# Kernel optimization log

Hardware: AMD Instinct MI355X
Metric: run time of the kernel (lower is better)

## Reference

```python
import jax, jax.numpy as jnp
import numpy as np

L, DIM = 8192, 2048

def setup_inputs() -> dict:
    key = jax.random.key(0)
    k1, k2, k3, k4 = jax.random.split(key, 4)
    x = jax.random.normal(k1, (L, DIM), dtype=jnp.float32)
    x_mix_last = jax.random.normal(k2, (DIM,), dtype=jnp.float32)
    factor_param = jax.random.uniform(k3, (DIM,), dtype=jnp.float32)
    W = jax.random.normal(k4, (DIM, DIM), dtype=jnp.float32) * 0.02
    return {"x": x, "x_mix_last": x_mix_last, "factor_param": factor_param, "W": W}

def reference(x, x_mix_last, factor_param, W):
    # x: [L, D] sequence-first, single sequence (no batch dim, as in the torch module)
    seq_len = x.shape[0]
    factor = jax.nn.sigmoid(factor_param)                       # [D]
    exps = jnp.arange(seq_len)[:, None]                         # [L, 1]
    factor_progression = factor[None, :] ** exps                # [L, D], factor^t
    n = 2 * seq_len
    # FFT-based causal convolution of x with the decay kernel factor^t
    fft_prog = jnp.fft.rfft(factor_progression, n=n, axis=0)    # [L+1, D] complex
    fft_x = jnp.fft.rfft(x, n=n, axis=0)                        # [L+1, D] complex
    conv = jnp.fft.irfft(fft_x * fft_prog, n=n, axis=0)[:seq_len]  # [L, D]
    # EMA update: carry decays as factor^(t+1), new input weighted by (1-factor)
    x_mix = x_mix_last[None, :] * factor_progression * factor[None, :] \
            + (1.0 - factor[None, :]) * conv                    # [L, D]
    return x_mix @ W.T                                          # nn.Linear: x @ W^T
```

## Files before the change

kernel.cpp:

```cpp
#include <hip/hip_runtime.h>

#define L_SEQ 8192
#define DIMN  2048
#define CHUNK 64
#define NCHUNK (L_SEQ / CHUNK)

typedef float  f32x4  __attribute__((ext_vector_type(4)));
typedef __bf16 bf16x8 __attribute__((ext_vector_type(8)));

__device__ __forceinline__ unsigned short f2bf(float f) {
    unsigned int u = __float_as_uint(f);
    u += 0x7fffu + ((u >> 16) & 1u);
    return (unsigned short)(u >> 16);
}

__device__ __forceinline__ float sigmoidf_(float v) {
    return 1.0f / (1.0f + __expf(-v));
}

__global__ void stage1(const float* __restrict__ x, const float* __restrict__ fp,
                       const float* __restrict__ W,
                       float* __restrict__ carry, unsigned short* __restrict__ Wb) {
    int b = blockIdx.x;
    if (b < 256) {
        int cg = b & 1;
        int c  = b >> 1;
        int d4 = cg * 256 + threadIdx.x;
        float4 f4 = ((const float4*)fp)[d4];
        float fa = sigmoidf_(f4.x), fb = sigmoidf_(f4.y),
              fc = sigmoidf_(f4.z), fd = sigmoidf_(f4.w);
        float ga = 1.f - fa, gb = 1.f - fb, gc = 1.f - fc, gd = 1.f - fd;
        float ha = 0.f, hb = 0.f, hc = 0.f, hd = 0.f;
        const float4* xp = (const float4*)(x + (size_t)c * CHUNK * DIMN) + d4;
#pragma unroll 8
        for (int t = 0; t < CHUNK; ++t) {
            float4 v = xp[(size_t)t * (DIMN / 4)];
            ha = fmaf(fa, ha, ga * v.x);
            hb = fmaf(fb, hb, gb * v.y);
            hc = fmaf(fc, hc, gc * v.z);
            hd = fmaf(fd, hd, gd * v.w);
        }
        ((float4*)(carry + (size_t)c * DIMN))[d4] = (float4){ha, hb, hc, hd};
    } else {
        int i = (b - 256) * 256 + threadIdx.x;
        float4 v = ((const float4*)W)[i];
        ushort4 o;
        o.x = f2bf(v.x); o.y = f2bf(v.y); o.z = f2bf(v.z); o.w = f2bf(v.w);
        ((ushort4*)Wb)[i] = o;
    }
}

__global__ void scan_apply(const float* __restrict__ x, const float* __restrict__ fp,
                           const float* __restrict__ xml, const float* __restrict__ carry,
                           unsigned short* __restrict__ xmix) {
    int b = blockIdx.x;
    int cg = b & 1;
    int c  = b >> 1;
    int d4 = cg * 256 + threadIdx.x;
    float4 f4 = ((const float4*)fp)[d4];
    float fa = sigmoidf_(f4.x), fb = sigmoidf_(f4.y),
          fc = sigmoidf_(f4.z), fd = sigmoidf_(f4.w);
    float ga = 1.f - fa, gb = 1.f - fb, gc = 1.f - fc, gd = 1.f - fd;

    float Fa = fa, Fb = fb, Fc = fc, Fd = fd;
    Fa *= Fa; Fa *= Fa; Fa *= Fa; Fa *= Fa; Fa *= Fa; Fa *= Fa;
    Fb *= Fb; Fb *= Fb; Fb *= Fb; Fb *= Fb; Fb *= Fb; Fb *= Fb;
    Fc *= Fc; Fc *= Fc; Fc *= Fc; Fc *= Fc; Fc *= Fc; Fc *= Fc;
    Fd *= Fd; Fd *= Fd; Fd *= Fd; Fd *= Fd; Fd *= Fd; Fd *= Fd;

    float4 m4 = ((const float4*)xml)[d4];
    float ha = m4.x, hb = m4.y, hc = m4.z, hd = m4.w;
    for (int j0 = 0; j0 < c; j0 += 16) {
        float4 v[16];
#pragma unroll
        for (int k = 0; k < 16; ++k)
            if (j0 + k < c)
                v[k] = ((const float4*)(carry + (size_t)(j0 + k) * DIMN))[d4];
#pragma unroll
        for (int k = 0; k < 16; ++k)
            if (j0 + k < c) {
                ha = fmaf(Fa, ha, v[k].x);
                hb = fmaf(Fb, hb, v[k].y);
                hc = fmaf(Fc, hc, v[k].z);
                hd = fmaf(Fd, hd, v[k].w);
            }
    }

    const float4* xp = (const float4*)(x + (size_t)c * CHUNK * DIMN) + d4;
    ushort4* op = (ushort4*)(xmix + (size_t)c * CHUNK * DIMN) + d4;
#pragma unroll 8
    for (int t = 0; t < CHUNK; ++t) {
        float4 v = xp[(size_t)t * (DIMN / 4)];
        ha = fmaf(fa, ha, ga * v.x);
        hb = fmaf(fb, hb, gb * v.y);
        hc = fmaf(fc, hc, gc * v.z);
        hd = fmaf(fd, hd, gd * v.w);
        ushort4 o; o.x = f2bf(ha); o.y = f2bf(hb); o.z = f2bf(hc); o.w = f2bf(hd);
        op[(size_t)t * (DIMN / 4)] = o;
    }
}

__global__ __launch_bounds__(256, 2) void gemm_bt(
        const unsigned short* __restrict__ A,
        const unsigned short* __restrict__ B,
        float* __restrict__ C) {
    constexpr int N_ = DIMN, K_ = DIMN;
    constexpr int BK = 64;
    __shared__ __align__(16) unsigned short As[128 * BK];
    __shared__ __align__(16) unsigned short Bs[256 * BK];

    int tid  = threadIdx.x;
    int wave = tid >> 6;
    int lane = tid & 63;
    int quad = lane >> 4;
    int l16  = lane & 15;
    int tm = blockIdx.x, tn = blockIdx.y;
    int wm = wave >> 1, wn = wave & 1;

    f32x4 acc[4][8];
#pragma unroll
    for (int i = 0; i < 4; ++i)
#pragma unroll
        for (int j = 0; j < 8; ++j)
            acc[i][j] = (f32x4){0.f, 0.f, 0.f, 0.f};

    const unsigned short* aBase = A + (size_t)(tm * 128) * K_;
    const unsigned short* bBase = B + (size_t)(tn * 256) * K_;

    for (int k0 = 0; k0 < K_; k0 += BK) {
#pragma unroll
        for (int i = 0; i < 4; ++i) {
            int idx = i * 256 + tid;
            int row = idx >> 3, slot = idx & 7;
            int cc = slot ^ (row & 7);
            __builtin_amdgcn_global_load_lds(
                (const __attribute__((address_space(1))) void*)(aBase + (size_t)row * K_ + k0 + cc * 8),
                (__attribute__((address_space(3))) void*)(As + idx * 8), 16, 0, 0);
        }
#pragma unroll
        for (int i = 0; i < 8; ++i) {
            int idx = i * 256 + tid;
            int row = idx >> 3, slot = idx & 7;
            int cc = slot ^ (row & 7);
            __builtin_amdgcn_global_load_lds(
                (const __attribute__((address_space(1))) void*)(bBase + (size_t)row * K_ + k0 + cc * 8),
                (__attribute__((address_space(3))) void*)(Bs + idx * 8), 16, 0, 0);
        }
        __syncthreads();

#pragma unroll
        for (int kk = 0; kk < BK; kk += 32) {
            bf16x8 af[4], bg[8];
#pragma unroll
            for (int i = 0; i < 4; ++i) {
                int r = wm * 64 + i * 16 + l16;
                int c0 = (kk >> 3) + quad;
                af[i] = *(const bf16x8*)(As + r * BK + ((c0 ^ (r & 7)) << 3));
            }
#pragma unroll
            for (int j = 0; j < 8; ++j) {
                int r = wn * 128 + j * 16 + l16;
                int c0 = (kk >> 3) + quad;
                bg[j] = *(const bf16x8*)(Bs + r * BK + ((c0 ^ (r & 7)) << 3));
            }
#pragma unroll
            for (int i = 0; i < 4; ++i)
#pragma unroll
                for (int j = 0; j < 8; ++j)
                    acc[i][j] = __builtin_amdgcn_mfma_f32_16x16x32_bf16(af[i], bg[j], acc[i][j], 0, 0, 0);
        }
        __syncthreads();
    }

#pragma unroll
    for (int i = 0; i < 4; ++i) {
#pragma unroll
        for (int j = 0; j < 8; ++j) {
            int col = tn * 256 + wn * 128 + j * 16 + l16;
#pragma unroll
            for (int r = 0; r < 4; ++r) {
                int row = tm * 128 + wm * 64 + i * 16 + quad * 4 + r;
                C[(size_t)row * N_ + col] = acc[i][j][r];
            }
        }
    }
}

extern "C" void kernel_launch(void* const* d_in, const int* in_sizes, int n_in,
                              void* d_out, int out_size, void* d_ws, size_t ws_size,
                              hipStream_t stream) {
    const float* x   = (const float*)d_in[0];
    const float* xml = (const float*)d_in[1];
    const float* fp  = (const float*)d_in[2];
    const float* W   = (const float*)d_in[3];
    float* out = (float*)d_out;

    unsigned short* xmix = (unsigned short*)d_ws;
    unsigned short* Wb   = (unsigned short*)((char*)d_ws + (size_t)L_SEQ * DIMN * 2);
    float* carry = (float*)((char*)d_ws + (size_t)L_SEQ * DIMN * 2 + (size_t)DIMN * DIMN * 2);

    stage1<<<256 + DIMN * DIMN / 4 / 256, 256, 0, stream>>>(x, fp, W, carry, Wb);
    scan_apply<<<256, 256, 0, stream>>>(x, fp, xml, carry, xmix);
    gemm_bt<<<dim3(L_SEQ / 128, DIMN / 256), 256, 0, stream>>>(xmix, Wb, out);
}
```

Before: 202.6 us.

## Fuse chunk scan phases into single-pass kernel with flag-based inter-block sync

```diff
diff --git a/kernel.cpp b/kernel.cpp
--- a/kernel.cpp
+++ b/kernel.cpp
@@ -2,8 +2,10 @@
 
 #define L_SEQ 8192
 #define DIMN  2048
-#define CHUNK 64
+#define CHUNK 32
 #define NCHUNK (L_SEQ / CHUNK)
+#define NSCAN  (2 * NCHUNK)
+#define NWCONV (DIMN * DIMN / 4 / 256)
 
 typedef float  f32x4  __attribute__((ext_vector_type(4)));
 typedef __bf16 bf16x8 __attribute__((ext_vector_type(8)));
@@ -18,67 +20,82 @@
     return 1.0f / (1.0f + __expf(-v));
 }
 
-__global__ void stage1(const float* __restrict__ x, const float* __restrict__ fp,
-                       const float* __restrict__ W,
-                       float* __restrict__ carry, unsigned short* __restrict__ Wb) {
-    int b = blockIdx.x;
-    if (b < 256) {
-        int cg = b & 1;
-        int c  = b >> 1;
-        int d4 = cg * 256 + threadIdx.x;
-        float4 f4 = ((const float4*)fp)[d4];
-        float fa = sigmoidf_(f4.x), fb = sigmoidf_(f4.y),
-              fc = sigmoidf_(f4.z), fd = sigmoidf_(f4.w);
-        float ga = 1.f - fa, gb = 1.f - fb, gc = 1.f - fc, gd = 1.f - fd;
+__global__ void zeroflags(unsigned int* __restrict__ flags) {
+    flags[threadIdx.x * 2]     = 0u;
+    flags[threadIdx.x * 2 + 1] = 0u;
+}
+
+__global__ __launch_bounds__(256) void scan1p(
+        const float* __restrict__ x, const float* __restrict__ fp,
+        const float* __restrict__ xml, const float* __restrict__ W,
+        float* __restrict__ carry, unsigned int* __restrict__ flags,
+        unsigned short* __restrict__ xmix, unsigned short* __restrict__ Wb) {
+    const int b   = blockIdx.x;
+    const int tid = threadIdx.x;
+
+    if (b >= NSCAN) {
+        int i = (b - NSCAN) * 256 + tid;
+        float4 v = ((const float4*)W)[i];
+        ushort4 o;
+        o.x = f2bf(v.x); o.y = f2bf(v.y); o.z = f2bf(v.z); o.w = f2bf(v.w);
+        ((ushort4*)Wb)[i] = o;
+        return;
+    }
+
+    const int cg = b & 1;
+    const int c  = b >> 1;
+    const int d4 = cg * 256 + tid;
+    float4 f4 = ((const float4*)fp)[d4];
+    float fa = sigmoidf_(f4.x), fb = sigmoidf_(f4.y),
+          fc = sigmoidf_(f4.z), fd = sigmoidf_(f4.w);
+    float ga = 1.f - fa, gb = 1.f - fb, gc = 1.f - fc, gd = 1.f - fd;
+
+    f32x4 loc[CHUNK];
+    const float4* xp = (const float4*)(x + (size_t)c * CHUNK * DIMN) + d4;
+    {
         float ha = 0.f, hb = 0.f, hc = 0.f, hd = 0.f;
-        const float4* xp = (const float4*)(x + (size_t)c * CHUNK * DIMN) + d4;
-#pragma unroll 8
+#pragma unroll
         for (int t = 0; t < CHUNK; ++t) {
             float4 v = xp[(size_t)t * (DIMN / 4)];
             ha = fmaf(fa, ha, ga * v.x);
             hb = fmaf(fb, hb, gb * v.y);
             hc = fmaf(fc, hc, gc * v.z);
             hd = fmaf(fd, hd, gd * v.w);
+            loc[t] = (f32x4){ha, hb, hc, hd};
         }
         ((float4*)(carry + (size_t)c * DIMN))[d4] = (float4){ha, hb, hc, hd};
-    } else {
-        int i = (b - 256) * 256 + threadIdx.x;
-        float4 v = ((const float4*)W)[i];
-        ushort4 o;
-        o.x = f2bf(v.x); o.y = f2bf(v.y); o.z = f2bf(v.z); o.w = f2bf(v.w);
-        ((ushort4*)Wb)[i] = o;
-    }
-}
-
-__global__ void scan_apply(const float* __restrict__ x, const float* __restrict__ fp,
-                           const float* __restrict__ xml, const float* __restrict__ carry,
-                           unsigned short* __restrict__ xmix) {
-    int b = blockIdx.x;
-    int cg = b & 1;
-    int c  = b >> 1;
-    int d4 = cg * 256 + threadIdx.x;
-    float4 f4 = ((const float4*)fp)[d4];
-    float fa = sigmoidf_(f4.x), fb = sigmoidf_(f4.y),
-          fc = sigmoidf_(f4.z), fd = sigmoidf_(f4.w);
-    float ga = 1.f - fa, gb = 1.f - fb, gc = 1.f - fc, gd = 1.f - fd;
+    }
+    __syncthreads();
+    if (tid == 0) {
+        __threadfence();
+        __hip_atomic_store(&flags[c * 2 + cg], 1u,
+                           __ATOMIC_RELEASE, __HIP_MEMORY_SCOPE_AGENT);
+    }
 
     float Fa = fa, Fb = fb, Fc = fc, Fd = fd;
-    Fa *= Fa; Fa *= Fa; Fa *= Fa; Fa *= Fa; Fa *= Fa; Fa *= Fa;
-    Fb *= Fb; Fb *= Fb; Fb *= Fb; Fb *= Fb; Fb *= Fb; Fb *= Fb;
-    Fc *= Fc; Fc *= Fc; Fc *= Fc; Fc *= Fc; Fc *= Fc; Fc *= Fc;
-    Fd *= Fd; Fd *= Fd; Fd *= Fd; Fd *= Fd; Fd *= Fd; Fd *= Fd;
-
+    Fa *= Fa; Fa *= Fa; Fa *= Fa; Fa *= Fa; Fa *= Fa;
+    Fb *= Fb; Fb *= Fb; Fb *= Fb; Fb *= Fb; Fb *= Fb;
+    Fc *= Fc; Fc *= Fc; Fc *= Fc; Fc *= Fc; Fc *= Fc;
+    Fd *= Fd; Fd *= Fd; Fd *= Fd; Fd *= Fd; Fd *= Fd;
     float4 m4 = ((const float4*)xml)[d4];
     float ha = m4.x, hb = m4.y, hc = m4.z, hd = m4.w;
     for (int j0 = 0; j0 < c; j0 += 16) {
+        int nb = c - j0; if (nb > 16) nb = 16;
+        if (tid < nb) {
+            while (__hip_atomic_load(&flags[(j0 + tid) * 2 + cg],
+                                     __ATOMIC_ACQUIRE, __HIP_MEMORY_SCOPE_AGENT) == 0u)
+                __builtin_amdgcn_s_sleep(1);
+        }
+        __syncthreads();
+        __threadfence();
         float4 v[16];
 #pragma unroll
         for (int k = 0; k < 16; ++k)
-            if (j0 + k < c)
+            if (k < nb)
                 v[k] = ((const float4*)(carry + (size_t)(j0 + k) * DIMN))[d4];
 #pragma unroll
         for (int k = 0; k < 16; ++k)
-            if (j0 + k < c) {
+            if (k < nb) {
                 ha = fmaf(Fa, ha, v[k].x);
                 hb = fmaf(Fb, hb, v[k].y);
                 hc = fmaf(Fc, hc, v[k].z);
@@ -86,17 +103,17 @@
             }
     }
 
-    const float4* xp = (const float4*)(x + (size_t)c * CHUNK * DIMN) + d4;
     ushort4* op = (ushort4*)(xmix + (size_t)c * CHUNK * DIMN) + d4;
-#pragma unroll 8
+    float pa = fa, pb = fb, pc = fc, pd = fd;
+#pragma unroll
     for (int t = 0; t < CHUNK; ++t) {
-        float4 v = xp[(size_t)t * (DIMN / 4)];
-        ha = fmaf(fa, ha, ga * v.x);
-        hb = fmaf(fb, hb, gb * v.y);
-        hc = fmaf(fc, hc, gc * v.z);
-        hd = fmaf(fd, hd, gd * v.w);
-        ushort4 o; o.x = f2bf(ha); o.y = f2bf(hb); o.z = f2bf(hc); o.w = f2bf(hd);
+        float oa = fmaf(pa, ha, loc[t][0]);
+        float ob = fmaf(pb, hb, loc[t][1]);
+        float oc = fmaf(pc, hc, loc[t][2]);
+        float od = fmaf(pd, hd, loc[t][3]);
+        ushort4 o; o.x = f2bf(oa); o.y = f2bf(ob); o.z = f2bf(oc); o.w = f2bf(od);
         op[(size_t)t * (DIMN / 4)] = o;
+        pa *= fa; pb *= fb; pc *= fc; pd *= fd;
     }
 }
 
@@ -197,9 +214,13 @@
 
     unsigned short* xmix = (unsigned short*)d_ws;
     unsigned short* Wb   = (unsigned short*)((char*)d_ws + (size_t)L_SEQ * DIMN * 2);
-    float* carry = (float*)((char*)d_ws + (size_t)L_SEQ * DIMN * 2 + (size_t)DIMN * DIMN * 2);
-
-    stage1<<<256 + DIMN * DIMN / 4 / 256, 256, 0, stream>>>(x, fp, W, carry, Wb);
-    scan_apply<<<256, 256, 0, stream>>>(x, fp, xml, carry, xmix);
+    float* carry = (float*)((char*)d_ws + (size_t)L_SEQ * DIMN * 2
+                                        + (size_t)DIMN * DIMN * 2);
+    unsigned int* flags = (unsigned int*)((char*)d_ws + (size_t)L_SEQ * DIMN * 2
+                                        + (size_t)DIMN * DIMN * 2
+                                        + (size_t)NCHUNK * DIMN * 4);
+
+    zeroflags<<<1, 256, 0, stream>>>(flags);
+    scan1p<<<NSCAN + NWCONV, 256, 0, stream>>>(x, fp, xml, W, carry, flags, xmix, Wb);
     gemm_bt<<<dim3(L_SEQ / 128, DIMN / 256), 256, 0, stream>>>(xmix, Wb, out);
 }
```

Measured after the change: 746.6 us. 268% more time.
